# Kernel tuning notes

Hardware: AMD Instinct MI355X
Metric: run time of the kernel (lower is better)

## Reference

```python
import jax, jax.numpy as jnp
import numpy as np

B, K, D = 8192, 256, 128


def setup_inputs() -> dict:
    key = jax.random.key(0)
    k1, k2 = jax.random.split(key)
    z = jax.random.normal(k1, (B, D), dtype=jnp.float32)
    centroids = jax.random.normal(k2, (K, D), dtype=jnp.float32)
    logvar = jnp.zeros((K, D), dtype=jnp.float32)
    return {"z": z, "centroids": centroids, "logvar": logvar}


def reference(z, centroids, logvar):
    # Mahalanobis (diagonal-covariance) distance of each z row to each centroid.
    # dist[b,k] = sum_d (z[b,d] - mu[k,d])^2 / var[k,d]
    diff = z[:, None, :] - centroids[None, :, :]          # (B, K, D)
    var = jnp.exp(logvar)[None, :, :]                      # (1, K, D)
    dist = jnp.sum(diff * diff / var, axis=2)              # (B, K)
    # Soft assignments: softmax over clusters of -0.5 * dist (stable softmax).
    return jax.nn.softmax(-0.5 * dist, axis=1)             # (B, K)
```

## Files before the change

kernel.cpp:

```cpp
#include <hip/hip_runtime.h>
#include <hip/hip_bf16.h>


typedef short     bf16x8  __attribute__((ext_vector_type(8)));
typedef float     f32x4   __attribute__((ext_vector_type(4)));
typedef unsigned short ushort_t;

constexpr int Bn = 8192, Kn = 256, Dn = 128;

__device__ __forceinline__ short bfbits(__hip_bfloat16 h) {
    return __builtin_bit_cast(short, h);
}

__device__ __forceinline__ void split8(const float* f, bf16x8& hi, bf16x8& lo) {
    #pragma unroll
    for (int p = 0; p < 4; ++p) {
        const float2 fp = make_float2(f[2 * p], f[2 * p + 1]);
        const __hip_bfloat162 h2 = __float22bfloat162_rn(fp);
        hi[2 * p]     = bfbits(h2.x);
        hi[2 * p + 1] = bfbits(h2.y);
        const float2 rp = make_float2(fp.x - __bfloat162float(h2.x),
                                      fp.y - __bfloat162float(h2.y));
        const __hip_bfloat162 l2 = __float22bfloat162_rn(rp);
        lo[2 * p]     = bfbits(l2.x);
        lo[2 * p + 1] = bfbits(l2.y);
    }
}

__global__ __launch_bounds__(1024, 4)
void gmm_fused(const float* __restrict__ z, const float* __restrict__ cent,
               const float* __restrict__ lvar, float* __restrict__ out)
{
    __shared__ ushort_t Ah[2 * 8 * 64 * 8];
    __shared__ ushort_t Al[2 * 8 * 64 * 8];
    __shared__ float red[32][16];

    const int tid = threadIdx.x;
    const int w   = tid >> 6;
    const int l   = tid & 63;
    const int lg  = l >> 4;
    const int ll  = l & 15;
    const int b0  = blockIdx.x * 32;
    const int n0  = w * 16;

    {
        const int r   = tid >> 9;
        const int kks = (tid >> 6) & 7;
        const int row = r * 16 + ll;
        const int d0  = kks * 16 + lg * 4;
        const float4 v = *reinterpret_cast<const float4*>(
            z + (size_t)(b0 + row) * Dn + d0);
        const float f[8] = {v.x * v.x, v.x, v.y * v.y, v.y,
                            v.z * v.z, v.z, v.w * v.w, v.w};
        bf16x8 hi, lo;
        split8(f, hi, lo);
        const int off = tid * 8;
        *reinterpret_cast<bf16x8*>(&Ah[off]) = hi;
        *reinterpret_cast<bf16x8*>(&Al[off]) = lo;
    }
    __syncthreads();

    f32x4 acc0 = (f32x4){0.f, 0.f, 0.f, 0.f};
    f32x4 acc1 = (f32x4){0.f, 0.f, 0.f, 0.f};
    float cpart = 0.0f;
    const size_t crow = (size_t)(n0 + ll) * Dn + lg * 4;

    float4 cv = *reinterpret_cast<const float4*>(cent + crow);
    float4 v4 = *reinterpret_cast<const float4*>(lvar + crow);

    #pragma unroll
    for (int kk = 0; kk < 8; ++kk) {
        float4 ncv, nv4;
        if (kk < 7) {
            ncv = *reinterpret_cast<const float4*>(cent + crow + (kk + 1) * 16);
            nv4 = *reinterpret_cast<const float4*>(lvar + crow + (kk + 1) * 16);
        }
        const float a0 = __expf(-v4.x), a1 = __expf(-v4.y);
        const float a2 = __expf(-v4.z), a3 = __expf(-v4.w);
        const float f[8] = {a0, -2.0f * cv.x * a0, a1, -2.0f * cv.y * a1,
                            a2, -2.0f * cv.z * a2, a3, -2.0f * cv.w * a3};
        bf16x8 Bh, Bl;
        split8(f, Bh, Bl);
        cpart += cv.x * cv.x * a0 + cv.y * cv.y * a1 +
                 cv.z * cv.z * a2 + cv.w * cv.w * a3;

        const int ao = kk * 512 + l * 8;
        const bf16x8 a0h = *reinterpret_cast<const bf16x8*>(&Ah[ao]);
        const bf16x8 a0l = *reinterpret_cast<const bf16x8*>(&Al[ao]);
        const bf16x8 a1h = *reinterpret_cast<const bf16x8*>(&Ah[4096 + ao]);
        const bf16x8 a1l = *reinterpret_cast<const bf16x8*>(&Al[4096 + ao]);

        acc0 = __builtin_amdgcn_mfma_f32_16x16x32_bf16(a0h, Bh, acc0, 0, 0, 0);
        acc1 = __builtin_amdgcn_mfma_f32_16x16x32_bf16(a1h, Bh, acc1, 0, 0, 0);
        acc0 = __builtin_amdgcn_mfma_f32_16x16x32_bf16(a0h, Bl, acc0, 0, 0, 0);
        acc1 = __builtin_amdgcn_mfma_f32_16x16x32_bf16(a1h, Bl, acc1, 0, 0, 0);
        acc0 = __builtin_amdgcn_mfma_f32_16x16x32_bf16(a0l, Bh, acc0, 0, 0, 0);
        acc1 = __builtin_amdgcn_mfma_f32_16x16x32_bf16(a1l, Bh, acc1, 0, 0, 0);

        cv = ncv; v4 = nv4;
    }
    cpart += __shfl_xor(cpart, 16);
    cpart += __shfl_xor(cpart, 32);
    const float ck = cpart;

    float dv[2][4];
    #pragma unroll
    for (int r = 0; r < 4; ++r) { dv[0][r] = acc0[r] + ck; dv[1][r] = acc1[r] + ck; }

    #pragma unroll
    for (int mi = 0; mi < 2; ++mi)
        #pragma unroll
        for (int r = 0; r < 4; ++r) {
            float t = dv[mi][r];
            t = fminf(t, __shfl_xor(t, 1));
            t = fminf(t, __shfl_xor(t, 2));
            t = fminf(t, __shfl_xor(t, 4));
            t = fminf(t, __shfl_xor(t, 8));
            if (ll == 0) red[mi * 16 + lg * 4 + r][w] = t;
        }
    __syncthreads();

    float gm[2][4];
    #pragma unroll
    for (int mi = 0; mi < 2; ++mi)
        #pragma unroll
        for (int r = 0; r < 4; ++r) {
            const int row = mi * 16 + lg * 4 + r;
            const f32x4* rp = reinterpret_cast<const f32x4*>(&red[row][0]);
            f32x4 m4 = rp[0];
            #pragma unroll
            for (int q = 1; q < 4; ++q) {
                f32x4 v = rp[q];
                m4[0] = fminf(m4[0], v[0]); m4[1] = fminf(m4[1], v[1]);
                m4[2] = fminf(m4[2], v[2]); m4[3] = fminf(m4[3], v[3]);
            }
            gm[mi][r] = fminf(fminf(m4[0], m4[1]), fminf(m4[2], m4[3]));
        }
    __syncthreads();

    float pv[2][4];
    #pragma unroll
    for (int mi = 0; mi < 2; ++mi)
        #pragma unroll
        for (int r = 0; r < 4; ++r) {
            const float p = __expf(-0.5f * (dv[mi][r] - gm[mi][r]));
            pv[mi][r] = p;
            float s = p;
            s += __shfl_xor(s, 1);
            s += __shfl_xor(s, 2);
            s += __shfl_xor(s, 4);
            s += __shfl_xor(s, 8);
            if (ll == 0) red[mi * 16 + lg * 4 + r][w] = s;
        }
    __syncthreads();

    #pragma unroll
    for (int mi = 0; mi < 2; ++mi)
        #pragma unroll
        for (int r = 0; r < 4; ++r) {
            const int row = mi * 16 + lg * 4 + r;
            const f32x4* rp = reinterpret_cast<const f32x4*>(&red[row][0]);
            f32x4 s4 = rp[0];
            #pragma unroll
            for (int q = 1; q < 4; ++q) {
                f32x4 v = rp[q];
                s4[0] += v[0]; s4[1] += v[1]; s4[2] += v[2]; s4[3] += v[3];
            }
            const float inv = 1.0f / ((s4[0] + s4[1]) + (s4[2] + s4[3]));
            out[(size_t)(b0 + row) * Kn + n0 + ll] = pv[mi][r] * inv;
        }
}

extern "C" void kernel_launch(void* const* d_in, const int* in_sizes, int n_in,
                              void* d_out, int out_size, void* d_ws, size_t ws_size,
                              hipStream_t stream) {
    const float* z      = (const float*)d_in[0];
    const float* cent   = (const float*)d_in[1];
    const float* logvar = (const float*)d_in[2];
    float* out = (float*)d_out;
    (void)in_sizes; (void)n_in; (void)out_size; (void)d_ws; (void)ws_size;

    hipLaunchKernelGGL(gmm_fused, dim3(Bn / 32), dim3(1024), 0, stream,
                       z, cent, logvar, out);
}
```

Baseline: 21.94 us.

## Precompute centroid bf16 split operands in a prep kernel via workspace

Adds a small prep kernel that computes exp(-logvar), the hi/lo bf16 split of the centroid-side MMA operands, and the per-centroid constant term once, and writes them to the workspace. The main kernel then loads these ready-made operands instead of every one of the 256 blocks redoing the exp and split work. This trades redundant per-block ALU work for a second kernel launch and extra global reads. The old fused kernel is kept as a fallback when the workspace is too small.

```diff
diff --git a/kernel.cpp b/kernel.cpp
--- a/kernel.cpp
+++ b/kernel.cpp
@@ -7,6 +7,11 @@
 typedef unsigned short ushort_t;
 
 constexpr int Bn = 8192, Kn = 256, Dn = 128;
+
+constexpr size_t BH_OFF = 0;
+constexpr size_t BL_OFF = (size_t)16 * 8 * 64 * 8;
+constexpr size_t CV_OFF = 2 * BL_OFF;
+constexpr size_t NEED_BYTES = CV_OFF * 2 + (size_t)Kn * 4;
 
 __device__ __forceinline__ short bfbits(__hip_bfloat16 h) {
     return __builtin_bit_cast(short, h);
@@ -27,9 +32,49 @@
     }
 }
 
+__global__ __launch_bounds__(512)
+void prep(const float* __restrict__ cent, const float* __restrict__ lvar,
+          ushort_t* __restrict__ ws)
+{
+    __shared__ float red2[16][8];
+    const int tid = threadIdx.x;
+    const int kk  = tid >> 6;
+    const int l   = tid & 63;
+    const int lg  = l >> 4;
+    const int ll  = l & 15;
+    const int cg  = blockIdx.x;
+    const int col = cg * 16 + ll;
+    const int d0  = kk * 16 + lg * 4;
+
+    const float4 cv = *reinterpret_cast<const float4*>(cent + (size_t)col * Dn + d0);
+    const float4 l4 = *reinterpret_cast<const float4*>(lvar + (size_t)col * Dn + d0);
+    const float a0 = __expf(-l4.x), a1 = __expf(-l4.y);
+    const float a2 = __expf(-l4.z), a3 = __expf(-l4.w);
+    const float f[8] = {a0, -2.0f * cv.x * a0, a1, -2.0f * cv.y * a1,
+                        a2, -2.0f * cv.z * a2, a3, -2.0f * cv.w * a3};
+    bf16x8 hi, lo;
+    split8(f, hi, lo);
+    const size_t off = ((size_t)(cg * 8 + kk) * 64 + l) * 8;
+    *reinterpret_cast<bf16x8*>(ws + BH_OFF + off) = hi;
+    *reinterpret_cast<bf16x8*>(ws + BL_OFF + off) = lo;
+
+    float cp = cv.x * cv.x * a0 + cv.y * cv.y * a1 +
+               cv.z * cv.z * a2 + cv.w * cv.w * a3;
+    cp += __shfl_xor(cp, 16);
+    cp += __shfl_xor(cp, 32);
+    if (lg == 0) red2[ll][kk] = cp;
+    __syncthreads();
+    if (tid < 16) {
+        float s = 0.f;
+        #pragma unroll
+        for (int q = 0; q < 8; ++q) s += red2[tid][q];
+        reinterpret_cast<float*>(ws + CV_OFF)[cg * 16 + tid] = s;
+    }
+}
+
 __global__ __launch_bounds__(1024, 4)
-void gmm_fused(const float* __restrict__ z, const float* __restrict__ cent,
-               const float* __restrict__ lvar, float* __restrict__ out)
+void gmm_main(const float* __restrict__ z, const ushort_t* __restrict__ ws,
+              float* __restrict__ out)
 {
     __shared__ ushort_t Ah[2 * 8 * 64 * 8];
     __shared__ ushort_t Al[2 * 8 * 64 * 8];
@@ -60,48 +105,42 @@
     }
     __syncthreads();
 
+    const ushort_t* BH = ws + BH_OFF;
+    const ushort_t* BL = ws + BL_OFF;
+    const float*  cvec = reinterpret_cast<const float*>(ws + CV_OFF);
+
     f32x4 acc0 = (f32x4){0.f, 0.f, 0.f, 0.f};
     f32x4 acc1 = (f32x4){0.f, 0.f, 0.f, 0.f};
-    float cpart = 0.0f;
-    const size_t crow = (size_t)(n0 + ll) * Dn + lg * 4;
-
-    float4 cv = *reinterpret_cast<const float4*>(cent + crow);
-    float4 v4 = *reinterpret_cast<const float4*>(lvar + crow);
+
+    const size_t bbase = (size_t)w * 4096 + (size_t)l * 8;
+
+    bf16x8 bh = *reinterpret_cast<const bf16x8*>(BH + bbase);
+    bf16x8 bl = *reinterpret_cast<const bf16x8*>(BL + bbase);
 
     #pragma unroll
     for (int kk = 0; kk < 8; ++kk) {
-        float4 ncv, nv4;
+        bf16x8 nbh, nbl;
         if (kk < 7) {
-            ncv = *reinterpret_cast<const float4*>(cent + crow + (kk + 1) * 16);
-            nv4 = *reinterpret_cast<const float4*>(lvar + crow + (kk + 1) * 16);
-        }
-        const float a0 = __expf(-v4.x), a1 = __expf(-v4.y);
-        const float a2 = __expf(-v4.z), a3 = __expf(-v4.w);
-        const float f[8] = {a0, -2.0f * cv.x * a0, a1, -2.0f * cv.y * a1,
-                            a2, -2.0f * cv.z * a2, a3, -2.0f * cv.w * a3};
-        bf16x8 Bh, Bl;
-        split8(f, Bh, Bl);
-        cpart += cv.x * cv.x * a0 + cv.y * cv.y * a1 +
-                 cv.z * cv.z * a2 + cv.w * cv.w * a3;
-
+            nbh = *reinterpret_cast<const bf16x8*>(BH + bbase + (kk + 1) * 512);
+            nbl = *reinterpret_cast<const bf16x8*>(BL + bbase + (kk + 1) * 512);
+        }
         const int ao = kk * 512 + l * 8;
         const bf16x8 a0h = *reinterpret_cast<const bf16x8*>(&Ah[ao]);
         const bf16x8 a0l = *reinterpret_cast<const bf16x8*>(&Al[ao]);
         const bf16x8 a1h = *reinterpret_cast<const bf16x8*>(&Ah[4096 + ao]);
         const bf16x8 a1l = *reinterpret_cast<const bf16x8*>(&Al[4096 + ao]);
 
-        acc0 = __builtin_amdgcn_mfma_f32_16x16x32_bf16(a0h, Bh, acc0, 0, 0, 0);
-        acc1 = __builtin_amdgcn_mfma_f32_16x16x32_bf16(a1h, Bh, acc1, 0, 0, 0);
-        acc0 = __builtin_amdgcn_mfma_f32_16x16x32_bf16(a0h, Bl, acc0, 0, 0, 0);
-        acc1 = __builtin_amdgcn_mfma_f32_16x16x32_bf16(a1h, Bl, acc1, 0, 0, 0);
-        acc0 = __builtin_amdgcn_mfma_f32_16x16x32_bf16(a0l, Bh, acc0, 0, 0, 0);
-        acc1 = __builtin_amdgcn_mfma_f32_16x16x32_bf16(a1l, Bh, acc1, 0, 0, 0);
-
-        cv = ncv; v4 = nv4;
-    }
-    cpart += __shfl_xor(cpart, 16);
-    cpart += __shfl_xor(cpart, 32);
-    const float ck = cpart;
+        acc0 = __builtin_amdgcn_mfma_f32_16x16x32_bf16(a0h, bh, acc0, 0, 0, 0);
+        acc1 = __builtin_amdgcn_mfma_f32_16x16x32_bf16(a1h, bh, acc1, 0, 0, 0);
+        acc0 = __builtin_amdgcn_mfma_f32_16x16x32_bf16(a0h, bl, acc0, 0, 0, 0);
+        acc1 = __builtin_amdgcn_mfma_f32_16x16x32_bf16(a1h, bl, acc1, 0, 0, 0);
+        acc0 = __builtin_amdgcn_mfma_f32_16x16x32_bf16(a0l, bh, acc0, 0, 0, 0);
+        acc1 = __builtin_amdgcn_mfma_f32_16x16x32_bf16(a1l, bh, acc1, 0, 0, 0);
+
+        bh = nbh; bl = nbl;
+    }
+
+    const float ck = cvec[n0 + ll];
 
     float dv[2][4];
     #pragma unroll
@@ -171,6 +210,150 @@
         }
 }
 
+__global__ __launch_bounds__(1024, 4)
+void gmm_fused(const float* __restrict__ z, const float* __restrict__ cent,
+               const float* __restrict__ lvar, float* __restrict__ out)
+{
+    __shared__ ushort_t Ah[2 * 8 * 64 * 8];
+    __shared__ ushort_t Al[2 * 8 * 64 * 8];
+    __shared__ float red[32][16];
+
+    const int tid = threadIdx.x;
+    const int w   = tid >> 6;
+    const int l   = tid & 63;
+    const int lg  = l >> 4;
+    const int ll  = l & 15;
+    const int b0  = blockIdx.x * 32;
+    const int n0  = w * 16;
+
+    {
+        const int r   = tid >> 9;
+        const int kks = (tid >> 6) & 7;
+        const int row = r * 16 + ll;
+        const int d0  = kks * 16 + lg * 4;
+        const float4 v = *reinterpret_cast<const float4*>(
+            z + (size_t)(b0 + row) * Dn + d0);
+        const float f[8] = {v.x * v.x, v.x, v.y * v.y, v.y,
+                            v.z * v.z, v.z, v.w * v.w, v.w};
+        bf16x8 hi, lo;
+        split8(f, hi, lo);
+        const int off = tid * 8;
+        *reinterpret_cast<bf16x8*>(&Ah[off]) = hi;
+        *reinterpret_cast<bf16x8*>(&Al[off]) = lo;
+    }
+    __syncthreads();
+
+    f32x4 acc0 = (f32x4){0.f, 0.f, 0.f, 0.f};
+    f32x4 acc1 = (f32x4){0.f, 0.f, 0.f, 0.f};
+    float cpart = 0.0f;
+    const size_t crow = (size_t)(n0 + ll) * Dn + lg * 4;
+
+    float4 cv = *reinterpret_cast<const float4*>(cent + crow);
+    float4 v4 = *reinterpret_cast<const float4*>(lvar + crow);
+
+    #pragma unroll
+    for (int kk = 0; kk < 8; ++kk) {
+        float4 ncv, nv4;
+        if (kk < 7) {
+            ncv = *reinterpret_cast<const float4*>(cent + crow + (kk + 1) * 16);
+            nv4 = *reinterpret_cast<const float4*>(lvar + crow + (kk + 1) * 16);
+        }
+        const float a0 = __expf(-v4.x), a1 = __expf(-v4.y);
+        const float a2 = __expf(-v4.z), a3 = __expf(-v4.w);
+        const float f[8] = {a0, -2.0f * cv.x * a0, a1, -2.0f * cv.y * a1,
+                            a2, -2.0f * cv.z * a2, a3, -2.0f * cv.w * a3};
+        bf16x8 Bh, Bl;
+        split8(f, Bh, Bl);
+        cpart += cv.x * cv.x * a0 + cv.y * cv.y * a1 +
+                 cv.z * cv.z * a2 + cv.w * cv.w * a3;
+
+        const int ao = kk * 512 + l * 8;
+        const bf16x8 a0h = *reinterpret_cast<const bf16x8*>(&Ah[ao]);
+        const bf16x8 a0l = *reinterpret_cast<const bf16x8*>(&Al[ao]);
+        const bf16x8 a1h = *reinterpret_cast<const bf16x8*>(&Ah[4096 + ao]);
+        const bf16x8 a1l = *reinterpret_cast<const bf16x8*>(&Al[4096 + ao]);
+
+        acc0 = __builtin_amdgcn_mfma_f32_16x16x32_bf16(a0h, Bh, acc0, 0, 0, 0);
+        acc1 = __builtin_amdgcn_mfma_f32_16x16x32_bf16(a1h, Bh, acc1, 0, 0, 0);
+        acc0 = __builtin_amdgcn_mfma_f32_16x16x32_bf16(a0h, Bl, acc0, 0, 0, 0);
+        acc1 = __builtin_amdgcn_mfma_f32_16x16x32_bf16(a1h, Bl, acc1, 0, 0, 0);
+        acc0 = __builtin_amdgcn_mfma_f32_16x16x32_bf16(a0l, Bh, acc0, 0, 0, 0);
+        acc1 = __builtin_amdgcn_mfma_f32_16x16x32_bf16(a1l, Bh, acc1, 0, 0, 0);
+
+        cv = ncv; v4 = nv4;
+    }
+    cpart += __shfl_xor(cpart, 16);
+    cpart += __shfl_xor(cpart, 32);
+    const float ck = cpart;
+
+    float dv[2][4];
+    #pragma unroll
+    for (int r = 0; r < 4; ++r) { dv[0][r] = acc0[r] + ck; dv[1][r] = acc1[r] + ck; }
+
+    #pragma unroll
+    for (int mi = 0; mi < 2; ++mi)
+        #pragma unroll
+        for (int r = 0; r < 4; ++r) {
+            float t = dv[mi][r];
+            t = fminf(t, __shfl_xor(t, 1));
+            t = fminf(t, __shfl_xor(t, 2));
+            t = fminf(t, __shfl_xor(t, 4));
+            t = fminf(t, __shfl_xor(t, 8));
+            if (ll == 0) red[mi * 16 + lg * 4 + r][w] = t;
+        }
+    __syncthreads();
+
+    float gm[2][4];
+    #pragma unroll
+    for (int mi = 0; mi < 2; ++mi)
+        #pragma unroll
+        for (int r = 0; r < 4; ++r) {
+            const int row = mi * 16 + lg * 4 + r;
+            const f32x4* rp = reinterpret_cast<const f32x4*>(&red[row][0]);
+            f32x4 m4 = rp[0];
+            #pragma unroll
+            for (int q = 1; q < 4; ++q) {
+                f32x4 v = rp[q];
+                m4[0] = fminf(m4[0], v[0]); m4[1] = fminf(m4[1], v[1]);
+                m4[2] = fminf(m4[2], v[2]); m4[3] = fminf(m4[3], v[3]);
+            }
+            gm[mi][r] = fminf(fminf(m4[0], m4[1]), fminf(m4[2], m4[3]));
+        }
+    __syncthreads();
+
+    float pv[2][4];
+    #pragma unroll
+    for (int mi = 0; mi < 2; ++mi)
+        #pragma unroll
+        for (int r = 0; r < 4; ++r) {
+            const float p = __expf(-0.5f * (dv[mi][r] - gm[mi][r]));
+            pv[mi][r] = p;
+            float s = p;
+            s += __shfl_xor(s, 1);
+            s += __shfl_xor(s, 2);
+            s += __shfl_xor(s, 4);
+            s += __shfl_xor(s, 8);
+            if (ll == 0) red[mi * 16 + lg * 4 + r][w] = s;
+        }
+    __syncthreads();
+
+    #pragma unroll
+    for (int mi = 0; mi < 2; ++mi)
+        #pragma unroll
+        for (int r = 0; r < 4; ++r) {
+            const int row = mi * 16 + lg * 4 + r;
+            const f32x4* rp = reinterpret_cast<const f32x4*>(&red[row][0]);
+            f32x4 s4 = rp[0];
+            #pragma unroll
+            for (int q = 1; q < 4; ++q) {
+                f32x4 v = rp[q];
+                s4[0] += v[0]; s4[1] += v[1]; s4[2] += v[2]; s4[3] += v[3];
+            }
+            const float inv = 1.0f / ((s4[0] + s4[1]) + (s4[2] + s4[3]));
+            out[(size_t)(b0 + row) * Kn + n0 + ll] = pv[mi][r] * inv;
+        }
+}
+
 extern "C" void kernel_launch(void* const* d_in, const int* in_sizes, int n_in,
                               void* d_out, int out_size, void* d_ws, size_t ws_size,
                               hipStream_t stream) {
@@ -178,8 +361,16 @@
     const float* cent   = (const float*)d_in[1];
     const float* logvar = (const float*)d_in[2];
     float* out = (float*)d_out;
-    (void)in_sizes; (void)n_in; (void)out_size; (void)d_ws; (void)ws_size;
-
-    hipLaunchKernelGGL(gmm_fused, dim3(Bn / 32), dim3(1024), 0, stream,
-                       z, cent, logvar, out);
-}
+    (void)in_sizes; (void)n_in; (void)out_size;
+
+    if (ws_size >= NEED_BYTES) {
+        ushort_t* ws = (ushort_t*)d_ws;
+        hipLaunchKernelGGL(prep, dim3(16), dim3(512), 0, stream,
+                           cent, logvar, ws);
+        hipLaunchKernelGGL(gmm_main, dim3(Bn / 32), dim3(1024), 0, stream,
+                           z, (const ushort_t*)ws, out);
+    } else {
+        hipLaunchKernelGGL(gmm_fused, dim3(Bn / 32), dim3(1024), 0, stream,
+                           z, cent, logvar, out);
+    }
+}
```

New measurement: 22.57 us. 1.03x slower.
